# Performance work log

Measured on AMD Instinct MI355X. Metric: run time of the kernel, lower is better.

The kernel has to match this reference:

```python
import jax, jax.numpy as jnp
import numpy as np

DEPTH = 2          # number of transformer blocks
DIM = 1280         # hidden_size
NHEADS = 16
HDIM = DIM // NHEADS  # 80
FF = 5120          # intermediate_size
S = 8192           # total ragged tokens
NSEG = 8           # number of image segments
EPS = 1e-6
GRID = 32          # per-image patch grid side (32*32*8 = 8192)


def _rotate_half(x):
    h = x.shape[-1] // 2
    return jnp.concatenate([-x[..., h:], x[..., :h]], axis=-1)


def _layernorm(x, g, b):
    mu = jnp.mean(x, axis=-1, keepdims=True)
    var = jnp.mean(jnp.square(x - mu), axis=-1, keepdims=True)
    return (x - mu) * jax.lax.rsqrt(var + EPS) * g + b


def setup_inputs() -> dict:
    key = jax.random.key(0)
    ks = jax.random.split(key, 16)
    std = 0.02
    hidden_states = jax.random.normal(ks[0], (S, DIM), jnp.float32)
    cu_seqlens = jnp.arange(NSEG + 1, dtype=jnp.int32) * (S // NSEG)
    # 2D rotary: per-axis freq table of size head_dim//4, concat row+col -> head_dim//2,
    # duplicated (cat(freqs, freqs)) -> head_dim, then cos/sin.
    rot_dim = HDIM // 2
    inv_freq = 1.0 / (10000.0 ** (jnp.arange(0, rot_dim, 2, dtype=jnp.float32) / rot_dim))  # [HDIM//4]
    tok = jnp.arange(S)
    rows = ((tok % (GRID * GRID)) // GRID).astype(jnp.float32)
    cols = (tok % GRID).astype(jnp.float32)
    freqs = jnp.concatenate([rows[:, None] * inv_freq[None, :], cols[:, None] * inv_freq[None, :]], axis=-1)  # [S, HDIM//2]
    emb = jnp.concatenate([freqs, freqs], axis=-1)  # [S, HDIM]
    cos = jnp.cos(emb)
    sin = jnp.sin(emb)
    def rnd(k, shape):
        return jax.random.normal(k, shape, jnp.float32) * std
    params = {
        'ln1_g': jnp.ones((DEPTH, DIM), jnp.float32), 'ln1_b': jnp.zeros((DEPTH, DIM), jnp.float32),
        'ln2_g': jnp.ones((DEPTH, DIM), jnp.float32), 'ln2_b': jnp.zeros((DEPTH, DIM), jnp.float32),
        'qkv_w': rnd(ks[1], (DEPTH, 3 * DIM, DIM)), 'qkv_b': jnp.zeros((DEPTH, 3 * DIM), jnp.float32),
        'proj_w': rnd(ks[2], (DEPTH, DIM, DIM)), 'proj_b': jnp.zeros((DEPTH, DIM), jnp.float32),
        'fc1_w': rnd(ks[3], (DEPTH, FF, DIM)), 'fc1_b': jnp.zeros((DEPTH, FF), jnp.float32),
        'fc2_w': rnd(ks[4], (DEPTH, DIM, FF)), 'fc2_b': jnp.zeros((DEPTH, DIM), jnp.float32),
    }
    return dict(hidden_states=hidden_states, cu_seqlens=cu_seqlens, cos=cos, sin=sin, **params)


def reference(hidden_states, cu_seqlens, cos, sin,
              ln1_g, ln1_b, ln2_g, ln2_b,
              qkv_w, qkv_b, proj_w, proj_b,
              fc1_w, fc1_b, fc2_w, fc2_b):
    seq = hidden_states.shape[0]
    # cu_seqlens is a static (int) input; derive the block-diagonal segmentation.
    seg = np.diff(np.asarray(jax.device_get(cu_seqlens)))
    L = int(seg[0])
    assert (seg == L).all(), 'reference assumes equal-length segments'
    n = len(seg)
    scale = HDIM ** -0.5
    c = cos[:, None, :]  # broadcast over heads, like cos.unsqueeze(1)
    s_ = sin[:, None, :]
    x = hidden_states
    for i in range(DEPTH):
        # --- attention ---
        h = _layernorm(x, ln1_g[i], ln1_b[i])
        qkv = (h @ qkv_w[i].T + qkv_b[i]).reshape(seq, 3, NHEADS, HDIM)
        q, k, v = qkv[:, 0], qkv[:, 1], qkv[:, 2]
        q = q * c + _rotate_half(q) * s_
        k = k * c + _rotate_half(k) * s_
        qs = q.reshape(n, L, NHEADS, HDIM)
        ks_ = k.reshape(n, L, NHEADS, HDIM)
        vs = v.reshape(n, L, NHEADS, HDIM)
        # block-diagonal (per-segment) attention, fp32 softmax
        attn = jnp.einsum('nlhd,nkhd->nhlk', qs, ks_) * scale
        p = jax.nn.softmax(attn, axis=-1)
        o = jnp.einsum('nhlk,nkhd->nlhd', p, vs).reshape(seq, DIM)
        x = x + (o @ proj_w[i].T + proj_b[i])
        # --- mlp (gelu tanh approx) ---
        h2 = _layernorm(x, ln2_g[i], ln2_b[i])
        x = x + (jax.nn.gelu(h2 @ fc1_w[i].T + fc1_b[i], approximate=True) @ fc2_w[i].T + fc2_b[i])
    return x
```

## Files before the change

kernel.cpp:

```cpp
#include <hip/hip_runtime.h>
#include <hip/hip_bf16.h>

typedef __attribute__((ext_vector_type(8))) short bf16x8;
typedef __attribute__((ext_vector_type(4))) float f32x4;
typedef __attribute__((ext_vector_type(8))) unsigned short u16x8;

__device__ __forceinline__ void gload_lds16(const void* g, void* l) {
  __builtin_amdgcn_global_load_lds(
      (const __attribute__((address_space(1))) unsigned int*)g,
      (__attribute__((address_space(3))) unsigned int*)l, 16, 0, 0);
}

__device__ __forceinline__ unsigned short f2bfu(float f) {
  __hip_bfloat16 h = __float2bfloat16(f);
  return __builtin_bit_cast(unsigned short, h);
}

__global__ __launch_bounds__(256) void copy_f32(const float* __restrict__ in,
                                                float* __restrict__ out, int n) {
  for (int i = blockIdx.x * 256 + threadIdx.x; i < n; i += gridDim.x * 256)
    out[i] = in[i];
}

__global__ __launch_bounds__(256) void w2bf(const float* __restrict__ in,
                                            __hip_bfloat16* __restrict__ out, int n) {
  for (int i = blockIdx.x * 256 + threadIdx.x; i < n; i += gridDim.x * 256)
    out[i] = __float2bfloat16(in[i]);
}

__global__ __launch_bounds__(256) void ln_kernel(const float* __restrict__ x,
                                                 const float* __restrict__ g,
                                                 const float* __restrict__ b,
                                                 __hip_bfloat16* __restrict__ h) {
  const int row = blockIdx.x;
  const int tid = threadIdx.x;
  const float* xr = x + (size_t)row * 1280;
  float v[5];
  float s = 0.f;
#pragma unroll
  for (int i = 0; i < 5; i++) { v[i] = xr[tid + i * 256]; s += v[i]; }
#pragma unroll
  for (int off = 32; off >= 1; off >>= 1) s += __shfl_xor(s, off);
  __shared__ float red[8];
  const int w = tid >> 6, lane = tid & 63;
  if (lane == 0) red[w] = s;
  __syncthreads();
  const float mu = (red[0] + red[1] + red[2] + red[3]) * (1.f / 1280.f);
  float q = 0.f;
#pragma unroll
  for (int i = 0; i < 5; i++) { float d = v[i] - mu; q += d * d; }
#pragma unroll
  for (int off = 32; off >= 1; off >>= 1) q += __shfl_xor(q, off);
  if (lane == 0) red[4 + w] = q;
  __syncthreads();
  const float var = (red[4] + red[5] + red[6] + red[7]) * (1.f / 1280.f);
  const float rstd = rsqrtf(var + 1e-6f);
#pragma unroll
  for (int i = 0; i < 5; i++) {
    int c = tid + i * 256;
    h[(size_t)row * 1280 + c] = __float2bfloat16((v[i] - mu) * rstd * g[c] + b[c]);
  }
}

__global__ __launch_bounds__(256) void rope_kernel(__hip_bfloat16* __restrict__ qkv,
                                                   const float* __restrict__ cs,
                                                   const float* __restrict__ sn) {
  const int TOT = 8192 * 2 * 16 * 40;
  for (int idx = blockIdx.x * 256 + threadIdx.x; idx < TOT; idx += gridDim.x * 256) {
    int d = idx % 40;
    int t = idx / 40;
    int head = t & 15;
    int t2 = t >> 4;
    int part = t2 & 1;
    int s = t2 >> 1;
    size_t base = ((size_t)s * 3 + part) * 1280 + head * 80;
    float e0 = __bfloat162float(qkv[base + d]);
    float e1 = __bfloat162float(qkv[base + d + 40]);
    float c0 = cs[s * 80 + d];
    float s0 = sn[s * 80 + d];
    float c1 = cs[s * 80 + d + 40];
    float s1 = sn[s * 80 + d + 40];
    qkv[base + d]      = __float2bfloat16(e0 * c0 - e1 * s0);
    qkv[base + d + 40] = __float2bfloat16(e1 * c1 + e0 * s1);
  }
}

__global__ __launch_bounds__(256) void vtrans_kernel(const __hip_bfloat16* __restrict__ qkv,
                                                     __hip_bfloat16* __restrict__ vt) {
  const int idx = blockIdx.x * 256 + threadIdx.x;
  const int s = idx & 8191;
  const int dc = idx >> 13;
  const unsigned short* src = (const unsigned short*)qkv + ((size_t)s * 3 + 2) * 1280 + dc * 8;
  u16x8 v = *(const u16x8*)src;
  unsigned short* dst = (unsigned short*)vt + (size_t)dc * 8 * 8192 + s;
#pragma unroll
  for (int j = 0; j < 8; j++) dst[(size_t)j * 8192] = v[j];
}

#define VMCNT4 asm volatile("s_waitcnt vmcnt(4)" ::: "memory")

#define GPHASE(MH, NH, DOA, STG, VM)                                                       \
  do {                                                                                     \
    if (DOA) {                                                                             \
      _Pragma("unroll") for (int mm = 0; mm < 4; mm++)                                     \
      _Pragma("unroll") for (int kk = 0; kk < 2; kk++)                                     \
        af[mm][kk] = *(const bf16x8*)(lds + bufOff + (MH) * 16384 + rowA + mm * 2048 + sw_s[kk]); \
    }                                                                                      \
    bf16x8 bfr[2][2];                                                                      \
    _Pragma("unroll") for (int nn = 0; nn < 2; nn++)                                       \
    _Pragma("unroll") for (int kk = 0; kk < 2; kk++)                                       \
      bfr[nn][kk] = *(const bf16x8*)(lds + bufOff + (NH) * 16384 + rowB + nn * 2048 + sw_s[kk]); \
    STG;                                                                                   \
    __builtin_amdgcn_s_barrier();                                                          \
    __builtin_amdgcn_s_setprio(1);                                                         \
    _Pragma("unroll") for (int kk = 0; kk < 2; kk++)                                       \
    _Pragma("unroll") for (int mm = 0; mm < 4; mm++)                                       \
    _Pragma("unroll") for (int nn = 0; nn < 2; nn++)                                       \
      acc[(MH) * 4 + mm][(NH) * 2 + nn] = __builtin_amdgcn_mfma_f32_16x16x32_bf16(         \
          af[mm][kk], bfr[nn][kk], acc[(MH) * 4 + mm][(NH) * 2 + nn], 0, 0, 0);            \
    __builtin_amdgcn_s_setprio(0);                                                         \
    VM;                                                                                    \
    __builtin_amdgcn_s_barrier();                                                          \
  } while (0)

template <int EPI>
__global__ __launch_bounds__(512, 2) void gemm256(const __hip_bfloat16* __restrict__ A,
                                                  const __hip_bfloat16* __restrict__ B,
                                                  const float* __restrict__ bias,
                                                  __hip_bfloat16* __restrict__ C,
                                                  float* __restrict__ X,
                                                  int M, int N, int K) {
  __shared__ __align__(16) char lds[131072];
  const int tid = threadIdx.x, lane = tid & 63, w = tid >> 6;
  const int wr = w >> 2, wc = w & 3;
  const int lm = lane & 15, hi = lane >> 4;

  const int nby = M >> 8, nbx = N >> 8;
  const int xcd = blockIdx.x & 7;
  const int local = blockIdx.x >> 3;
  const int by = xcd * (nby >> 3) + local / nbx;
  const int bx = local % nbx;
  const long mBase = (long)by << 8, nBase = (long)bx << 8;

  f32x4 acc[8][4];
#pragma unroll
  for (int m = 0; m < 8; m++)
#pragma unroll
    for (int n = 0; n < 4; n++) acc[m][n] = (f32x4){0.f, 0.f, 0.f, 0.f};

  const int r0 = (w << 3) + (lane >> 3);
  const int slotT = (lane & 7) ^ (lane >> 3);
  const unsigned short* Ag = (const unsigned short*)A;
  const unsigned short* Bg = (const unsigned short*)B;
  const size_t aB = (size_t)(mBase + r0) * K + slotT * 8;
  const size_t bB = (size_t)(nBase + r0) * K + slotT * 8;
  const int wdst = w << 10;

  auto STAGE = [&](int tile, int half, int isB) {
    char* dst = lds + ((tile & 1) << 16) + (isB << 15) + (half << 14) + wdst;
    const unsigned short* src =
        (isB ? Bg + bB : Ag + aB) + (size_t)(half << 7) * (size_t)K + ((size_t)tile << 6);
    gload_lds16(src, dst);
    gload_lds16(src + ((size_t)K << 6), dst + 8192);
  };

  const int rowA = (wr * 64 + lm) * 128;
  const int rowB = (wc * 32 + lm) * 128 + 32768;
  const int key = lm & 7;
  int sw_s[2];
#pragma unroll
  for (int kk = 0; kk < 2; kk++) sw_s[kk] = (((kk << 2) | hi) ^ key) << 4;

  const int nt = K >> 6;

  STAGE(0, 0, 0); STAGE(0, 0, 1); STAGE(0, 1, 1); STAGE(0, 1, 0);
  STAGE(1, 0, 0); STAGE(1, 0, 1);
  VMCNT4;
  __builtin_amdgcn_s_barrier();

  for (int t = 0; t < nt; ++t) {
    const int bufOff = (t & 1) << 16;
    const bool s1 = t + 1 < nt, s2 = t + 2 < nt;
    bf16x8 af[4][2];
    GPHASE(0, 0, 1, if (s1) STAGE(t + 1, 1, 1), (void)0);
    GPHASE(0, 1, 0, if (s1) STAGE(t + 1, 1, 0), (void)0);
    GPHASE(1, 0, 1, if (s2) STAGE(t + 2, 0, 0), (void)0);
    GPHASE(1, 1, 0, if (s2) STAGE(t + 2, 0, 1), VMCNT4);
  }

#pragma unroll
  for (int n = 0; n < 4; n++) {
    const int col = (int)nBase + (n >> 1) * 128 + wc * 32 + (n & 1) * 16 + lm;
    const float bv = bias[col];
#pragma unroll
    for (int m = 0; m < 8; m++) {
      const int er = (int)mBase + (m >> 2) * 128 + wr * 64 + (m & 3) * 16 + hi * 4;
#pragma unroll
      for (int j = 0; j < 4; j++) {
        float v = acc[m][n][j] + bv;
        size_t off = (size_t)(er + j) * N + col;
        if constexpr (EPI == 0) {
          C[off] = __float2bfloat16(v);
        } else if constexpr (EPI == 1) {
          float u = v + 0.044715f * v * v * v;
          float E = exp2f(2.30220818f * u);
          float t = 1.f - 2.f / (E + 1.f);
          C[off] = __float2bfloat16(0.5f * v * (1.f + t));
        } else {
          X[off] += v;
        }
      }
    }
  }
}

__global__ __launch_bounds__(256) void attn_kernel(const __hip_bfloat16* __restrict__ qkv,
                                                   const __hip_bfloat16* __restrict__ vtg,
                                                   __hip_bfloat16* __restrict__ o) {
  __shared__ __align__(16) unsigned short Ks[64 * 96];
  __shared__ __align__(16) unsigned short Vt[80 * 72];
  __shared__ __align__(16) unsigned short Ps[4][16 * 68];
  const int tid = threadIdx.x, lane = tid & 63, w = tid >> 6;
  const int lm = lane & 15, hi = lane >> 4;
  const int qt = blockIdx.x, head = blockIdx.y, seg = blockIdx.z;
  const int s0 = seg * 1024;
  const int qrow0 = s0 + qt * 64;
  const unsigned short* qg = (const unsigned short*)qkv;
  const unsigned short* vg = (const unsigned short*)vtg + (size_t)head * 80 * 8192;

  for (int idx = tid; idx < 1024; idx += 256) {
    int r = idx >> 4, c = 80 + (idx & 15);
    Ks[r * 96 + c] = 0;
  }

  bf16x8 aq[3];
  {
    const unsigned short* qrow = qg + (size_t)(qrow0 + w * 16 + lm) * 3840 + head * 80;
#pragma unroll
    for (int kk = 0; kk < 3; kk++) aq[kk] = *(const bf16x8*)(qrow + kk * 32 + hi * 8);
  }

  auto loadKV = [&](int kt, u16x8* kr, u16x8* vr) {
#pragma unroll
    for (int it = 0; it < 3; it++) {
      int c = tid + it * 256;
      if (c < 640) {
        int r = c / 10, c8 = c % 10;
        kr[it] = *(const u16x8*)(qg + ((size_t)(s0 + kt * 64 + r) * 3 + 1) * 1280 +
                                 head * 80 + c8 * 8);
        int d = c >> 3, sc = c & 7;
        vr[it] = *(const u16x8*)(vg + (size_t)d * 8192 + s0 + kt * 64 + sc * 8);
      }
    }
  };
  auto writeKV = [&](u16x8* kr, u16x8* vr) {
#pragma unroll
    for (int it = 0; it < 3; it++) {
      int c = tid + it * 256;
      if (c < 640) {
        int r = c / 10, c8 = c % 10;
        *(u16x8*)&Ks[r * 96 + c8 * 8] = kr[it];
        int d = c >> 3, sc = c & 7;
        *(u16x8*)&Vt[d * 72 + sc * 8] = vr[it];
      }
    }
  };

  {
    u16x8 kr[3], vr[3];
    loadKV(0, kr, vr);
    writeKV(kr, vr);
  }
  __syncthreads();

  float m_s[4] = {-1e30f, -1e30f, -1e30f, -1e30f};
  float l_s[4] = {0.f, 0.f, 0.f, 0.f};
  f32x4 accO[5];
#pragma unroll
  for (int nf = 0; nf < 5; nf++) accO[nf] = (f32x4){0.f, 0.f, 0.f, 0.f};

  const float SM = 0.11180339887498949f * 1.4426950408889634f;

  for (int kt = 0; kt < 16; kt++) {
    u16x8 krn[3], vrn[3];
    if (kt + 1 < 16) loadKV(kt + 1, krn, vrn);

    f32x4 sf[4];
#pragma unroll
    for (int n = 0; n < 4; n++) sf[n] = (f32x4){0.f, 0.f, 0.f, 0.f};
#pragma unroll
    for (int kk = 0; kk < 3; kk++) {
#pragma unroll
      for (int n = 0; n < 4; n++) {
        bf16x8 bk = *(const bf16x8*)(&Ks[(n * 16 + lm) * 96 + kk * 32 + hi * 8]);
        sf[n] = __builtin_amdgcn_mfma_f32_16x16x32_bf16(aq[kk], bk, sf[n], 0, 0, 0);
      }
    }

    float alpha[4];
#pragma unroll
    for (int j = 0; j < 4; j++) {
      float v = fmaxf(fmaxf(sf[0][j], sf[1][j]), fmaxf(sf[2][j], sf[3][j]));
#pragma unroll
      for (int off = 1; off < 16; off <<= 1) v = fmaxf(v, __shfl_xor(v, off));
      float mn = fmaxf(m_s[j], v);
      alpha[j] = exp2f((m_s[j] - mn) * SM);
      m_s[j] = mn;
    }
    float rsum[4] = {0.f, 0.f, 0.f, 0.f};
#pragma unroll
    for (int n = 0; n < 4; n++)
#pragma unroll
      for (int j = 0; j < 4; j++) {
        float p = exp2f((sf[n][j] - m_s[j]) * SM);
        sf[n][j] = p;
        rsum[j] += p;
      }
#pragma unroll
    for (int j = 0; j < 4; j++) {
#pragma unroll
      for (int off = 1; off < 16; off <<= 1) rsum[j] += __shfl_xor(rsum[j], off);
      l_s[j] = l_s[j] * alpha[j] + rsum[j];
    }
#pragma unroll
    for (int nf = 0; nf < 5; nf++)
#pragma unroll
      for (int j = 0; j < 4; j++) accO[nf][j] *= alpha[j];

#pragma unroll
    for (int n = 0; n < 4; n++)
#pragma unroll
      for (int j = 0; j < 4; j++)
        Ps[w][(hi * 4 + j) * 68 + n * 16 + lm] = f2bfu(sf[n][j]);

#pragma unroll
    for (int kk = 0; kk < 2; kk++) {
      bf16x8 pa = *(const bf16x8*)(&Ps[w][lm * 68 + kk * 32 + hi * 8]);
#pragma unroll
      for (int nf = 0; nf < 5; nf++) {
        bf16x8 bv = *(const bf16x8*)(&Vt[(nf * 16 + lm) * 72 + kk * 32 + hi * 8]);
        accO[nf] = __builtin_amdgcn_mfma_f32_16x16x32_bf16(pa, bv, accO[nf], 0, 0, 0);
      }
    }

    __syncthreads();
    if (kt + 1 < 16) writeKV(krn, vrn);
    __syncthreads();
  }

#pragma unroll
  for (int nf = 0; nf < 5; nf++) {
    int d = nf * 16 + lm;
#pragma unroll
    for (int j = 0; j < 4; j++) {
      int r = qrow0 + w * 16 + hi * 4 + j;
      o[(size_t)r * 1280 + head * 80 + d] = __float2bfloat16(accO[nf][j] / l_s[j]);
    }
  }
}

extern "C" void kernel_launch(void* const* d_in, const int* in_sizes, int n_in,
                              void* d_out, int out_size, void* d_ws, size_t ws_size,
                              hipStream_t stream) {
  (void)in_sizes; (void)n_in; (void)out_size; (void)ws_size;
  const float* hidden = (const float*)d_in[0];
  const float* cs   = (const float*)d_in[2];
  const float* sn   = (const float*)d_in[3];
  const float* ln1g = (const float*)d_in[4];
  const float* ln1b = (const float*)d_in[5];
  const float* ln2g = (const float*)d_in[6];
  const float* ln2b = (const float*)d_in[7];
  const float* qkvw = (const float*)d_in[8];
  const float* qkvb = (const float*)d_in[9];
  const float* pw   = (const float*)d_in[10];
  const float* pb   = (const float*)d_in[11];
  const float* f1w  = (const float*)d_in[12];
  const float* f1b  = (const float*)d_in[13];
  const float* f2w  = (const float*)d_in[14];
  const float* f2b  = (const float*)d_in[15];

  float* x = (float*)d_out;

  char* ws = (char*)d_ws;
  __hip_bfloat16* h    = (__hip_bfloat16*)ws;
  __hip_bfloat16* vt   = (__hip_bfloat16*)ws;
  __hip_bfloat16* qkv  = (__hip_bfloat16*)(ws + 20971520);
  __hip_bfloat16* o    = (__hip_bfloat16*)(ws + 83886080);
  __hip_bfloat16* ffh  = (__hip_bfloat16*)(ws + 20971520);
  __hip_bfloat16* wbuf = (__hip_bfloat16*)(ws + 104857600);

  const int NTOK = 8192 * 1280;
  copy_f32<<<2048, 256, 0, stream>>>(hidden, x, NTOK);
  for (int i = 0; i < 2; i++) {
    ln_kernel<<<8192, 256, 0, stream>>>(x, ln1g + i * 1280, ln1b + i * 1280, h);

    w2bf<<<2048, 256, 0, stream>>>(qkvw + (size_t)i * 3840 * 1280, wbuf, 3840 * 1280);
    gemm256<0><<<480, 512, 0, stream>>>(h, wbuf, qkvb + i * 3840, qkv, nullptr,
                                        8192, 3840, 1280);
    vtrans_kernel<<<5120, 256, 0, stream>>>(qkv, vt);
    rope_kernel<<<4096, 256, 0, stream>>>(qkv, cs, sn);
    attn_kernel<<<dim3(16, 16, 8), 256, 0, stream>>>(qkv, vt, o);

    w2bf<<<2048, 256, 0, stream>>>(pw + (size_t)i * 1280 * 1280, wbuf, 1280 * 1280);
    gemm256<2><<<160, 512, 0, stream>>>(o, wbuf, pb + i * 1280, nullptr, x,
                                        8192, 1280, 1280);

    ln_kernel<<<8192, 256, 0, stream>>>(x, ln2g + i * 1280, ln2b + i * 1280, h);

    w2bf<<<2048, 256, 0, stream>>>(f1w + (size_t)i * 5120 * 1280, wbuf, 5120 * 1280);
    gemm256<1><<<640, 512, 0, stream>>>(h, wbuf, f1b + i * 5120, ffh, nullptr,
                                        8192, 5120, 1280);

    w2bf<<<2048, 256, 0, stream>>>(f2w + (size_t)i * 1280 * 5120, wbuf, 1280 * 5120);
    gemm256<2><<<160, 512, 0, stream>>>(ffh, wbuf, f2b + i * 1280, nullptr, x,
                                        8192, 1280, 5120);
  }
}
```

Measured before the change: 1.392 ms.

## Preload GEMM B fragments per K-step and enlarge attention tiles to 128

```diff
diff --git a/kernel.cpp b/kernel.cpp
--- a/kernel.cpp
+++ b/kernel.cpp
@@ -99,29 +99,15 @@
 
 #define VMCNT4 asm volatile("s_waitcnt vmcnt(4)" ::: "memory")
 
-#define GPHASE(MH, NH, DOA, STG, VM)                                                       \
-  do {                                                                                     \
-    if (DOA) {                                                                             \
-      _Pragma("unroll") for (int mm = 0; mm < 4; mm++)                                     \
-      _Pragma("unroll") for (int kk = 0; kk < 2; kk++)                                     \
-        af[mm][kk] = *(const bf16x8*)(lds + bufOff + (MH) * 16384 + rowA + mm * 2048 + sw_s[kk]); \
-    }                                                                                      \
-    bf16x8 bfr[2][2];                                                                      \
-    _Pragma("unroll") for (int nn = 0; nn < 2; nn++)                                       \
-    _Pragma("unroll") for (int kk = 0; kk < 2; kk++)                                       \
-      bfr[nn][kk] = *(const bf16x8*)(lds + bufOff + (NH) * 16384 + rowB + nn * 2048 + sw_s[kk]); \
-    STG;                                                                                   \
-    __builtin_amdgcn_s_barrier();                                                          \
-    __builtin_amdgcn_s_setprio(1);                                                         \
-    _Pragma("unroll") for (int kk = 0; kk < 2; kk++)                                       \
-    _Pragma("unroll") for (int mm = 0; mm < 4; mm++)                                       \
-    _Pragma("unroll") for (int nn = 0; nn < 2; nn++)                                       \
-      acc[(MH) * 4 + mm][(NH) * 2 + nn] = __builtin_amdgcn_mfma_f32_16x16x32_bf16(         \
-          af[mm][kk], bfr[nn][kk], acc[(MH) * 4 + mm][(NH) * 2 + nn], 0, 0, 0);            \
-    __builtin_amdgcn_s_setprio(0);                                                         \
-    VM;                                                                                    \
-    __builtin_amdgcn_s_barrier();                                                          \
-  } while (0)
+#define MFMAQ(MH, NH)                                                                      \
+  __builtin_amdgcn_s_barrier();                                                            \
+  __builtin_amdgcn_s_setprio(1);                                                           \
+  _Pragma("unroll") for (int kk = 0; kk < 2; kk++)                                         \
+  _Pragma("unroll") for (int mm = 0; mm < 4; mm++)                                         \
+  _Pragma("unroll") for (int nn = 0; nn < 2; nn++)                                         \
+    acc[(MH) * 4 + mm][(NH) * 2 + nn] = __builtin_amdgcn_mfma_f32_16x16x32_bf16(           \
+        af[mm][kk], bq[NH][nn][kk], acc[(MH) * 4 + mm][(NH) * 2 + nn], 0, 0, 0);           \
+  __builtin_amdgcn_s_setprio(0);
 
 template <int EPI>
 __global__ __launch_bounds__(512, 2) void gemm256(const __hip_bfloat16* __restrict__ A,
@@ -181,11 +167,38 @@
   for (int t = 0; t < nt; ++t) {
     const int bufOff = (t & 1) << 16;
     const bool s1 = t + 1 < nt, s2 = t + 2 < nt;
-    bf16x8 af[4][2];
-    GPHASE(0, 0, 1, if (s1) STAGE(t + 1, 1, 1), (void)0);
-    GPHASE(0, 1, 0, if (s1) STAGE(t + 1, 1, 0), (void)0);
-    GPHASE(1, 0, 1, if (s2) STAGE(t + 2, 0, 0), (void)0);
-    GPHASE(1, 1, 0, if (s2) STAGE(t + 2, 0, 1), VMCNT4);
+    bf16x8 af[4][2], bq[2][2][2];
+#pragma unroll
+    for (int mm = 0; mm < 4; mm++)
+#pragma unroll
+      for (int kk = 0; kk < 2; kk++)
+        af[mm][kk] = *(const bf16x8*)(lds + bufOff + rowA + mm * 2048 + sw_s[kk]);
+#pragma unroll
+    for (int nh = 0; nh < 2; nh++)
+#pragma unroll
+      for (int nn = 0; nn < 2; nn++)
+#pragma unroll
+        for (int kk = 0; kk < 2; kk++)
+          bq[nh][nn][kk] =
+              *(const bf16x8*)(lds + bufOff + nh * 16384 + rowB + nn * 2048 + sw_s[kk]);
+    if (s1) STAGE(t + 1, 1, 1);
+    MFMAQ(0, 0);
+    __builtin_amdgcn_s_barrier();
+    if (s1) STAGE(t + 1, 1, 0);
+    MFMAQ(0, 1);
+    __builtin_amdgcn_s_barrier();
+#pragma unroll
+    for (int mm = 0; mm < 4; mm++)
+#pragma unroll
+      for (int kk = 0; kk < 2; kk++)
+        af[mm][kk] = *(const bf16x8*)(lds + bufOff + 16384 + rowA + mm * 2048 + sw_s[kk]);
+    if (s2) STAGE(t + 2, 0, 0);
+    MFMAQ(1, 0);
+    __builtin_amdgcn_s_barrier();
+    if (s2) STAGE(t + 2, 0, 1);
+    MFMAQ(1, 1);
+    VMCNT4;
+    __builtin_amdgcn_s_barrier();
   }
 
 #pragma unroll
@@ -204,8 +217,8 @@
         } else if constexpr (EPI == 1) {
           float u = v + 0.044715f * v * v * v;
           float E = exp2f(2.30220818f * u);
-          float t = 1.f - 2.f / (E + 1.f);
-          C[off] = __float2bfloat16(0.5f * v * (1.f + t));
+          float t2 = 1.f - 2.f / (E + 1.f);
+          C[off] = __float2bfloat16(0.5f * v * (1.f + t2));
         } else {
           X[off] += v;
         }
@@ -214,21 +227,21 @@
   }
 }
 
-__global__ __launch_bounds__(256) void attn_kernel(const __hip_bfloat16* __restrict__ qkv,
-                                                   const __hip_bfloat16* __restrict__ vtg,
-                                                   __hip_bfloat16* __restrict__ o) {
-  __shared__ __align__(16) unsigned short Ks[64 * 96];
-  __shared__ __align__(16) unsigned short Vt[80 * 72];
-  __shared__ __align__(16) unsigned short Ps[4][16 * 68];
+__global__ __launch_bounds__(512, 4) void attn_kernel(const __hip_bfloat16* __restrict__ qkv,
+                                                      const __hip_bfloat16* __restrict__ vtg,
+                                                      __hip_bfloat16* __restrict__ o) {
+  __shared__ __align__(16) unsigned short Ks[128 * 96];
+  __shared__ __align__(16) unsigned short Vt[80 * 136];
+  __shared__ __align__(16) unsigned short Ps[8][16 * 68];
   const int tid = threadIdx.x, lane = tid & 63, w = tid >> 6;
   const int lm = lane & 15, hi = lane >> 4;
   const int qt = blockIdx.x, head = blockIdx.y, seg = blockIdx.z;
   const int s0 = seg * 1024;
-  const int qrow0 = s0 + qt * 64;
+  const int qrow0 = s0 + qt * 128;
   const unsigned short* qg = (const unsigned short*)qkv;
   const unsigned short* vg = (const unsigned short*)vtg + (size_t)head * 80 * 8192;
 
-  for (int idx = tid; idx < 1024; idx += 256) {
+  for (int idx = tid; idx < 2048; idx += 512) {
     int r = idx >> 4, c = 80 + (idx & 15);
     Ks[r * 96 + c] = 0;
   }
@@ -243,25 +256,25 @@
   auto loadKV = [&](int kt, u16x8* kr, u16x8* vr) {
 #pragma unroll
     for (int it = 0; it < 3; it++) {
-      int c = tid + it * 256;
-      if (c < 640) {
+      int c = tid + it * 512;
+      if (c < 1280) {
         int r = c / 10, c8 = c % 10;
-        kr[it] = *(const u16x8*)(qg + ((size_t)(s0 + kt * 64 + r) * 3 + 1) * 1280 +
+        kr[it] = *(const u16x8*)(qg + ((size_t)(s0 + kt * 128 + r) * 3 + 1) * 1280 +
                                  head * 80 + c8 * 8);
-        int d = c >> 3, sc = c & 7;
-        vr[it] = *(const u16x8*)(vg + (size_t)d * 8192 + s0 + kt * 64 + sc * 8);
+        int d = c >> 4, sc = c & 15;
+        vr[it] = *(const u16x8*)(vg + (size_t)d * 8192 + s0 + kt * 128 + sc * 8);
       }
     }
   };
   auto writeKV = [&](u16x8* kr, u16x8* vr) {
 #pragma unroll
     for (int it = 0; it < 3; it++) {
-      int c = tid + it * 256;
-      if (c < 640) {
+      int c = tid + it * 512;
+      if (c < 1280) {
         int r = c / 10, c8 = c % 10;
         *(u16x8*)&Ks[r * 96 + c8 * 8] = kr[it];
-        int d = c >> 3, sc = c & 7;
-        *(u16x8*)&Vt[d * 72 + sc * 8] = vr[it];
+        int d = c >> 4, sc = c & 15;
+        *(u16x8*)&Vt[d * 136 + sc * 8] = vr[it];
       }
     }
   };
@@ -281,17 +294,17 @@
 
   const float SM = 0.11180339887498949f * 1.4426950408889634f;
 
-  for (int kt = 0; kt < 16; kt++) {
+  for (int kt = 0; kt < 8; kt++) {
     u16x8 krn[3], vrn[3];
-    if (kt + 1 < 16) loadKV(kt + 1, krn, vrn);
-
-    f32x4 sf[4];
-#pragma unroll
-    for (int n = 0; n < 4; n++) sf[n] = (f32x4){0.f, 0.f, 0.f, 0.f};
+    if (kt + 1 < 8) loadKV(kt + 1, krn, vrn);
+
+    f32x4 sf[8];
+#pragma unroll
+    for (int n = 0; n < 8; n++) sf[n] = (f32x4){0.f, 0.f, 0.f, 0.f};
 #pragma unroll
     for (int kk = 0; kk < 3; kk++) {
 #pragma unroll
-      for (int n = 0; n < 4; n++) {
+      for (int n = 0; n < 8; n++) {
         bf16x8 bk = *(const bf16x8*)(&Ks[(n * 16 + lm) * 96 + kk * 32 + hi * 8]);
         sf[n] = __builtin_amdgcn_mfma_f32_16x16x32_bf16(aq[kk], bk, sf[n], 0, 0, 0);
       }
@@ -300,7 +313,9 @@
     float alpha[4];
 #pragma unroll
     for (int j = 0; j < 4; j++) {
-      float v = fmaxf(fmaxf(sf[0][j], sf[1][j]), fmaxf(sf[2][j], sf[3][j]));
+      float v = sf[0][j];
+#pragma unroll
+      for (int n = 1; n < 8; n++) v = fmaxf(v, sf[n][j]);
 #pragma unroll
       for (int off = 1; off < 16; off <<= 1) v = fmaxf(v, __shfl_xor(v, off));
       float mn = fmaxf(m_s[j], v);
@@ -309,7 +324,7 @@
     }
     float rsum[4] = {0.f, 0.f, 0.f, 0.f};
 #pragma unroll
-    for (int n = 0; n < 4; n++)
+    for (int n = 0; n < 8; n++)
 #pragma unroll
       for (int j = 0; j < 4; j++) {
         float p = exp2f((sf[n][j] - m_s[j]) * SM);
@@ -328,23 +343,26 @@
       for (int j = 0; j < 4; j++) accO[nf][j] *= alpha[j];
 
 #pragma unroll
-    for (int n = 0; n < 4; n++)
-#pragma unroll
-      for (int j = 0; j < 4; j++)
-        Ps[w][(hi * 4 + j) * 68 + n * 16 + lm] = f2bfu(sf[n][j]);
-
-#pragma unroll
-    for (int kk = 0; kk < 2; kk++) {
-      bf16x8 pa = *(const bf16x8*)(&Ps[w][lm * 68 + kk * 32 + hi * 8]);
-#pragma unroll
-      for (int nf = 0; nf < 5; nf++) {
-        bf16x8 bv = *(const bf16x8*)(&Vt[(nf * 16 + lm) * 72 + kk * 32 + hi * 8]);
-        accO[nf] = __builtin_amdgcn_mfma_f32_16x16x32_bf16(pa, bv, accO[nf], 0, 0, 0);
+    for (int h = 0; h < 2; h++) {
+#pragma unroll
+      for (int n = 0; n < 4; n++)
+#pragma unroll
+        for (int j = 0; j < 4; j++)
+          Ps[w][(hi * 4 + j) * 68 + n * 16 + lm] = f2bfu(sf[h * 4 + n][j]);
+#pragma unroll
+      for (int kk = 0; kk < 2; kk++) {
+        bf16x8 pa = *(const bf16x8*)(&Ps[w][lm * 68 + kk * 32 + hi * 8]);
+#pragma unroll
+        for (int nf = 0; nf < 5; nf++) {
+          bf16x8 bv =
+              *(const bf16x8*)(&Vt[(nf * 16 + lm) * 136 + h * 64 + kk * 32 + hi * 8]);
+          accO[nf] = __builtin_amdgcn_mfma_f32_16x16x32_bf16(pa, bv, accO[nf], 0, 0, 0);
+        }
       }
     }
 
     __syncthreads();
-    if (kt + 1 < 16) writeKV(krn, vrn);
+    if (kt + 1 < 8) writeKV(krn, vrn);
     __syncthreads();
   }
 
@@ -399,7 +417,7 @@
                                         8192, 3840, 1280);
     vtrans_kernel<<<5120, 256, 0, stream>>>(qkv, vt);
     rope_kernel<<<4096, 256, 0, stream>>>(qkv, cs, sn);
-    attn_kernel<<<dim3(16, 16, 8), 256, 0, stream>>>(qkv, vt, o);
+    attn_kernel<<<dim3(8, 16, 8), 512, 0, stream>>>(qkv, vt, o);
 
     w2bf<<<2048, 256, 0, stream>>>(pw + (size_t)i * 1280 * 1280, wbuf, 1280 * 1280);
     gemm256<2><<<160, 512, 0, stream>>>(o, wbuf, pb + i * 1280, nullptr, x,
```

New measurement: 1.367 ms. No clear change (-1.8%).
